# Kernel optimization log

Measured on AMD Instinct MI355X. Metric: run time of the kernel, lower is better.

## Reference

```python
import jax, jax.numpy as jnp
import numpy as np
import math

N_HEAD = 9
N_KV_HEAD = 3
HEAD_DIM = 64
ROPE_THETA = 100000.0


def _rope_cos_sin(seq_len, dim, theta):
    inv_freq = 1.0 / (theta ** (jnp.arange(0, dim, 2, dtype=jnp.float32) / dim))  # (dim//2,)
    t = jnp.arange(seq_len, dtype=jnp.float32)
    ang = jnp.outer(t, inv_freq)  # (T, dim//2)
    return jnp.cos(ang), jnp.sin(ang)


def _apply_rope(x, cos, sin):
    # x: (B, H, T, D); pairs are interleaved along D (torch view_as_complex on (..., D//2, 2))
    B, H, T, D = x.shape
    xr = x.reshape(B, H, T, D // 2, 2)
    x0, x1 = xr[..., 0], xr[..., 1]
    c = cos[None, None, :, :]
    s = sin[None, None, :, :]
    out0 = x0 * c - x1 * s
    out1 = x0 * s + x1 * c
    return jnp.stack([out0, out1], axis=-1).reshape(B, H, T, D)


def setup_inputs() -> dict:
    key = jax.random.key(0)
    ks = jax.random.split(key, 5)
    B, T, C = 4, 2048, 576
    scale_in = 1.0 / math.sqrt(C)
    return {
        "x": jax.random.normal(ks[0], (B, T, C), dtype=jnp.float32),
        "wq": jax.random.normal(ks[1], (N_HEAD * HEAD_DIM, C), dtype=jnp.float32) * scale_in,
        "wk": jax.random.normal(ks[2], (N_KV_HEAD * HEAD_DIM, C), dtype=jnp.float32) * scale_in,
        "wv": jax.random.normal(ks[3], (N_KV_HEAD * HEAD_DIM, C), dtype=jnp.float32) * scale_in,
        "wo": jax.random.normal(ks[4], (C, N_HEAD * HEAD_DIM), dtype=jnp.float32) * scale_in,
    }


def reference(x, wq, wk, wv, wo):
    B, T, C = x.shape
    n_rep = N_HEAD // N_KV_HEAD

    q = (x @ wq.T).reshape(B, T, N_HEAD, HEAD_DIM).transpose(0, 2, 1, 3)      # (B,Hq,T,D)
    k = (x @ wk.T).reshape(B, T, N_KV_HEAD, HEAD_DIM).transpose(0, 2, 1, 3)   # (B,Hkv,T,D)
    v = (x @ wv.T).reshape(B, T, N_KV_HEAD, HEAD_DIM).transpose(0, 2, 1, 3)

    cos, sin = _rope_cos_sin(T, HEAD_DIM, ROPE_THETA)
    q = _apply_rope(q, cos, sin)
    k = _apply_rope(k, cos, sin)

    # GQA: broadcast each KV head across n_rep query heads without materializing copies
    qg = q.reshape(B, N_KV_HEAD, n_rep, T, HEAD_DIM)
    att = jnp.einsum("bgrtd,bgsd->bgrts", qg, k) * (1.0 / math.sqrt(HEAD_DIM))  # (B,Hkv,rep,T,T)
    causal = jnp.tril(jnp.ones((T, T), dtype=bool))
    att = jnp.where(causal[None, None, None, :, :], att, -jnp.inf)
    att = jax.nn.softmax(att, axis=-1)
    y = jnp.einsum("bgrts,bgsd->bgrtd", att, v)                                # (B,Hkv,rep,T,D)
    y = y.reshape(B, N_HEAD, T, HEAD_DIM).transpose(0, 2, 1, 3).reshape(B, T, N_HEAD * HEAD_DIM)
    return y @ wo.T
```

## Files before the change

kernel.cpp:

```cpp
#include <hip/hip_runtime.h>
#include <stdint.h>

typedef __attribute__((ext_vector_type(8))) short bf16x8;
typedef __attribute__((ext_vector_type(16))) float f32x16;

#define MFMA32(a, b, c) __builtin_amdgcn_mfma_f32_32x32x16_bf16(a, b, c, 0, 0, 0)

#define BB 4
#define TT 2048
#define CC 576
#define NH 9
#define NKV 3
#define HD 64
#define MM (BB * TT)
#define NQKV 960

#define QSC 0.18033688011112042f

__device__ __forceinline__ unsigned short f2bf(float f) {
  union { float f; uint32_t u; } v; v.f = f;
  uint32_t u = v.u;
  uint32_t r = (u + 0x7fffu + ((u >> 16) & 1u)) >> 16;
  return (unsigned short)r;
}

__device__ __forceinline__ void gl16(const void* g, void* l) {
  __builtin_amdgcn_global_load_lds(
      (const __attribute__((address_space(1))) unsigned int*)g,
      (__attribute__((address_space(3))) unsigned int*)l, 16, 0, 0);
}

__device__ __forceinline__ float fexp2(float x) {
  float r;
  asm("v_exp_f32 %0, %1" : "=v"(r) : "v"(x));
  return r;
}

__global__ __launch_bounds__(256) void prep_kernel(
    const float* __restrict__ x, const float* __restrict__ wq,
    const float* __restrict__ wk, const float* __restrict__ wv,
    const float* __restrict__ wo,
    unsigned short* __restrict__ xh, unsigned short* __restrict__ wqkv,
    unsigned short* __restrict__ woh, float* __restrict__ tc,
    float* __restrict__ ts) {
  const int NX4 = MM * CC / 4;
  const int NW4 = NQKV * CC / 4;
  const int NO4 = CC * CC / 4;
  const int NT = TT * 32;
  const int total = NX4 + NW4 + NO4 + NT;
  for (int i = blockIdx.x * blockDim.x + threadIdx.x; i < total;
       i += gridDim.x * blockDim.x) {
    if (i < NX4) {
      float4 v = ((const float4*)x)[i];
      ushort4 o;
      o.x = f2bf(v.x); o.y = f2bf(v.y); o.z = f2bf(v.z); o.w = f2bf(v.w);
      ((ushort4*)xh)[i] = o;
    } else if (i < NX4 + NW4) {
      int j = i - NX4;
      int n = (j * 4) / CC;
      const float* src = (n < 576) ? wq + j * 4
                       : (n < 768) ? wk + j * 4 - 576 * CC
                                   : wv + j * 4 - 768 * CC;
      float4 v = *(const float4*)src;
      ushort4 o;
      o.x = f2bf(v.x); o.y = f2bf(v.y); o.z = f2bf(v.z); o.w = f2bf(v.w);
      ((ushort4*)wqkv)[j] = o;
    } else if (i < NX4 + NW4 + NO4) {
      int j = i - NX4 - NW4;
      float4 v = ((const float4*)wo)[j];
      ushort4 o;
      o.x = f2bf(v.x); o.y = f2bf(v.y); o.z = f2bf(v.z); o.w = f2bf(v.w);
      ((ushort4*)woh)[j] = o;
    } else {
      int j = i - NX4 - NW4 - NO4;
      int t = j >> 5, pi = j & 31;
      double invf = pow(100000.0, -(double)(2 * pi) / 64.0);
      double ang = (double)t * invf;
      tc[j] = (float)cos(ang);
      ts[j] = (float)sin(ang);
    }
  }
}

__global__ __launch_bounds__(512, 4) void gemm_qkv(
    const unsigned short* __restrict__ xh, const unsigned short* __restrict__ wqkv,
    const float* __restrict__ tc, const float* __restrict__ ts,
    unsigned short* __restrict__ qb, unsigned short* __restrict__ kst,
    unsigned short* __restrict__ vst) {
  const int l = threadIdx.x & 63, w = threadIdx.x >> 6;
  const int ln = l & 31, hi = l >> 5;
  const int bm = blockIdx.y * 256, bn = blockIdx.x * 64;

  __shared__ unsigned short als[2][16384];
  __shared__ unsigned short bls[2][4096];

  int asrc[4];
#pragma unroll
  for (int i = 0; i < 4; ++i)
    asrc[i] = (bm + w * 32 + i * 8 + (l >> 3)) * CC + ((l & 7) ^ ((l >> 3) & 7)) * 8;
  const int bsrc = (bn + w * 8 + (l >> 3)) * CC + ((l & 7) ^ ((l >> 3) & 7)) * 8;

  f32x16 acc0, acc1;
#pragma unroll
  for (int r = 0; r < 16; ++r) { acc0[r] = 0.f; acc1[r] = 0.f; }

#pragma unroll
  for (int i = 0; i < 4; ++i) gl16(xh + asrc[i], (char*)&als[0][0] + w * 4096 + i * 1024);
  gl16(wqkv + bsrc, (char*)&bls[0][0] + w * 1024);

  int cur = 0;
  for (int t = 0; t < 9; ++t) {
    if (t + 1 < 9) {
      const int k0 = (t + 1) * 64;
#pragma unroll
      for (int i = 0; i < 4; ++i)
        gl16(xh + asrc[i] + k0, (char*)&als[cur ^ 1][0] + w * 4096 + i * 1024);
      gl16(wqkv + bsrc + k0, (char*)&bls[cur ^ 1][0] + w * 1024);
      asm volatile("s_waitcnt vmcnt(5)" ::: "memory");
    } else {
      asm volatile("s_waitcnt vmcnt(0)" ::: "memory");
    }
    __builtin_amdgcn_s_barrier();
    __builtin_amdgcn_sched_barrier(0);

    const char* ab = (const char*)&als[cur][0];
    const char* bb = (const char*)&bls[cur][0];
    __builtin_amdgcn_s_setprio(1);
#pragma unroll
    for (int ks = 0; ks < 4; ++ks) {
      const int ch = (((ks * 2 + hi) ^ (ln & 7)) << 4);
      bf16x8 af = *(const bf16x8*)(ab + (w * 32 + ln) * 128 + ch);
      bf16x8 b0 = *(const bf16x8*)(bb + ln * 128 + ch);
      bf16x8 b1 = *(const bf16x8*)(bb + (32 + ln) * 128 + ch);
      acc0 = MFMA32(af, b0, acc0);
      acc1 = MFMA32(af, b1, acc1);
    }
    __builtin_amdgcn_s_setprio(0);

    __builtin_amdgcn_sched_barrier(0);
    __builtin_amdgcn_s_barrier();
    cur ^= 1;
  }

#pragma unroll
  for (int n32 = 0; n32 < 2; ++n32) {
    const int col = bn + n32 * 32 + ln;
    const int d = col & 63;
#pragma unroll
    for (int r = 0; r < 16; ++r) {
      const int m = bm + w * 32 + (r & 3) + 8 * (r >> 2) + 4 * hi;
      float v = n32 ? acc1[r] : acc0[r];
      float partner = __shfl_xor(v, 1);
      const int bi = m >> 11, t = m & 2047;
      if (col < 768) {
        const int pi = d >> 1;
        const float c = tc[t * 32 + pi], s = ts[t * 32 + pi];
        v = (d & 1) ? (partner * s + v * c) : (v * c - partner * s);
      }
      if (col < 576) {
        const int h = col >> 6;
        qb[(((size_t)bi * NH + h) * TT + t) * HD + d] = f2bf(v * QSC);
      } else if (col < 768) {
        const int h = (col - 576) >> 6;
        const size_t head = (size_t)bi * NKV + h;
        const int tt = t & 63;
        kst[(head * 32 + (t >> 6)) * 4096 + ((d >> 4) * 2 + (tt >> 5)) * 512
            + ((((d >> 3) & 1) << 5) + (tt & 31)) * 8 + (d & 7)] = f2bf(v);
      } else {
        const int h = (col - 768) >> 6;
        const size_t head = (size_t)bi * NKV + h;
        const int tt = t & 63;
        vst[(head * 32 + (t >> 6)) * 4096 + ((tt >> 4) * 2 + (d >> 5)) * 512
            + ((((tt >> 3) & 1) << 5) + (d & 31)) * 8 + (tt & 7)] = f2bf(v);
      }
    }
  }
}

__global__ __launch_bounds__(512) void attn_kernel(
    const unsigned short* __restrict__ qbuf, const unsigned short* __restrict__ kst,
    const unsigned short* __restrict__ vst, unsigned short* __restrict__ yb) {
  const int j = blockIdx.x, kvh = blockIdx.y, b = blockIdx.z;
  const int i = j % 7, hr = j / 7;
  const int h = kvh * 3 + hr;
  const int l = threadIdx.x & 63;
  const int w8 = threadIdx.x >> 6;
  const int g = w8 >> 2;
  const int wq = w8 & 3;
  const int ln = l & 31, hi = l >> 5;
  const size_t head = (size_t)b * NKV + kvh;

  const int qt0 = 15 - i, qt1 = i + 2, qt2 = (i == 5) ? 0 : 1;
  const int m0 = qt0 + 1, m1 = qt1 + 1;
  const int m2 = (i >= 5) ? qt2 + 1 : 0;
  const int m01 = m0 + m1;
  const int tot = m01 + m2;

  __shared__ unsigned short kls[2][3][4096];
  __shared__ unsigned short vls[2][3][4096];
  __shared__ float licomb[256];

  const unsigned short* qptr = qbuf + ((size_t)b * NH + h) * TT * HD;
  const int row0 = qt0 * 128 + wq * 32 + ln;
  const int row1 = qt1 * 128 + wq * 32 + ln;
  const int row2 = qt2 * 128 + wq * 32 + ln;

  bf16x8 qf0[4], qf1[4], qf2[4], qc[4];
#pragma unroll
  for (int ds = 0; ds < 4; ++ds) {
    qf0[ds] = *(const bf16x8*)(qptr + (size_t)row0 * HD + ds * 16 + hi * 8);
    qf1[ds] = *(const bf16x8*)(qptr + (size_t)row1 * HD + ds * 16 + hi * 8);
    qf2[ds] = *(const bf16x8*)(qptr + (size_t)row2 * HD + ds * 16 + hi * 8);
  }
  qc[0] = qf0[0]; qc[1] = qf0[1]; qc[2] = qf0[2]; qc[3] = qf0[3];
  int qt_c = qt0, qrow_c = row0, nt_c = m0;

  const char* kgb = (const char*)(kst + head * 32 * 4096);
  const char* vgb = (const char*)(vst + head * 32 * 4096);

  f32x16 o0, o1, fzero;
  float ls[16];
#pragma unroll
  for (int r = 0; r < 16; ++r) { o0[r] = 0.f; o1[r] = 0.f; ls[r] = 0.f; fzero[r] = 0.f; }

#pragma unroll
  for (int pre = 0; pre < 2; ++pre) {
    const size_t tb = (size_t)(2 * pre + g) * 8192;
#pragma unroll
    for (int i2 = 0; i2 < 2; ++i2) {
      const int off = wq * 2048 + i2 * 1024;
      gl16(kgb + tb + off + l * 16, (char*)&kls[g][pre][0] + off);
      gl16(vgb + tb + off + l * 16, (char*)&vls[g][pre][0] + off);
    }
  }
  asm volatile("s_waitcnt vmcnt(4)" ::: "memory");
  __builtin_amdgcn_s_barrier();
  __builtin_amdgcn_sched_barrier(0);

  int jt = 0;
  int s = 0;

  for (int it = 0; it < tot; ++it) {
    if (it + 2 < tot) {
      const int f = it + 2;
      const int u2 = (f < m0) ? f : ((f < m01) ? f - m0 : f - m01);
      const size_t tb = (size_t)(2 * u2 + g) * 8192;
      char* kl = (char*)&kls[g][(it + 2) % 3][0];
      char* vl = (char*)&vls[g][(it + 2) % 3][0];
#pragma unroll
      for (int i2 = 0; i2 < 2; ++i2) {
        const int off = wq * 2048 + i2 * 1024;
        gl16(kgb + tb + off + l * 16, kl + off);
        gl16(vgb + tb + off + l * 16, vl + off);
      }
    }

    const char* kb = (const char*)&kls[g][it % 3][0];
    const char* vb = (const char*)&vls[g][it % 3][0];

    f32x16 s0, s1;
    __builtin_amdgcn_s_setprio(1);
    {
      bf16x8 k0 = *(const bf16x8*)(kb + 0 * 1024 + l * 16);
      bf16x8 k1 = *(const bf16x8*)(kb + 1 * 1024 + l * 16);
      s0 = MFMA32(k0, qc[0], fzero);
      s1 = MFMA32(k1, qc[0], fzero);
    }
#pragma unroll
    for (int ds = 1; ds < 4; ++ds) {
      bf16x8 k0 = *(const bf16x8*)(kb + (ds * 2 + 0) * 1024 + l * 16);
      bf16x8 k1 = *(const bf16x8*)(kb + (ds * 2 + 1) * 1024 + l * 16);
      s0 = MFMA32(k0, qc[ds], s0);
      s1 = MFMA32(k1, qc[ds], s1);
    }
    __builtin_amdgcn_s_setprio(0);

    const bool segEnd = (jt == qt_c);
    if (segEnd) {
      const int kvt = 2 * qt_c + g;
#pragma unroll
      for (int r = 0; r < 16; ++r) {
        const int kg = kvt * 64 + (r & 3) + 8 * (r >> 2) + 4 * hi;
        if (kg > qrow_c) s0[r] = -1e30f;
        if (kg + 32 > qrow_c) s1[r] = -1e30f;
      }
    }

#pragma unroll
    for (int r = 0; r < 16; ++r) {
      s0[r] = fexp2(s0[r]);
      s1[r] = fexp2(s1[r]);
    }
#pragma unroll
    for (int r = 0; r < 16; ++r) ls[r] += s0[r] + s1[r];

    unsigned int pa[4][4];
#pragma unroll
    for (int t = 0; t < 2; ++t) {
#pragma unroll
      for (int m = 0; m < 2; ++m) {
        float p0 = t ? s1[8 * m + 0] : s0[8 * m + 0];
        float p1 = t ? s1[8 * m + 1] : s0[8 * m + 1];
        float p2 = t ? s1[8 * m + 2] : s0[8 * m + 2];
        float p3 = t ? s1[8 * m + 3] : s0[8 * m + 3];
        float p4 = t ? s1[8 * m + 4] : s0[8 * m + 4];
        float p5 = t ? s1[8 * m + 5] : s0[8 * m + 5];
        float p6 = t ? s1[8 * m + 6] : s0[8 * m + 6];
        float p7 = t ? s1[8 * m + 7] : s0[8 * m + 7];
        unsigned int w0, w1, w2, w3;
        asm("v_cvt_pk_bf16_f32 %0, %1, %2" : "=v"(w0) : "v"(p0), "v"(p1));
        asm("v_cvt_pk_bf16_f32 %0, %1, %2" : "=v"(w1) : "v"(p2), "v"(p3));
        asm("v_cvt_pk_bf16_f32 %0, %1, %2" : "=v"(w2) : "v"(p4), "v"(p5));
        asm("v_cvt_pk_bf16_f32 %0, %1, %2" : "=v"(w3) : "v"(p6), "v"(p7));
        asm("v_permlane32_swap_b32 %0, %1" : "+v"(w0), "+v"(w2));
        asm("v_permlane32_swap_b32 %0, %1" : "+v"(w1), "+v"(w3));
        pa[2 * t + m][0] = w0; pa[2 * t + m][1] = w1;
        pa[2 * t + m][2] = w2; pa[2 * t + m][3] = w3;
      }
    }

    __builtin_amdgcn_s_setprio(1);
#pragma unroll
    for (int ks = 0; ks < 4; ++ks) {
      union { unsigned int u[4]; bf16x8 v; } cvt;
      cvt.u[0] = pa[ks][0]; cvt.u[1] = pa[ks][1];
      cvt.u[2] = pa[ks][2]; cvt.u[3] = pa[ks][3];
      bf16x8 v0 = *(const bf16x8*)(vb + (ks * 2 + 0) * 1024 + l * 16);
      bf16x8 v1 = *(const bf16x8*)(vb + (ks * 2 + 1) * 1024 + l * 16);
      o0 = MFMA32(cvt.v, v0, o0);
      o1 = MFMA32(cvt.v, v1, o1);
    }
    __builtin_amdgcn_s_setprio(0);

    if (segEnd) {
#pragma unroll
      for (int st = 8; st >= 1; st >>= 1)
#pragma unroll
        for (int r = 0; r < 8; ++r)
          if (r < st) ls[r] += ls[r + st];
      const float tm0 = ls[0] + __shfl_xor(ls[0], 32);
      char* chunk;
      {
        const int buf = it % 3;
        chunk = (char*)((wq == 0) ? &kls[0][buf][0]
               : (wq == 1) ? &vls[0][buf][0]
               : (wq == 2) ? &kls[1][buf][0]
                           : &vls[1][buf][0]);
      }
      __syncthreads();
      if (g == 1) {
#pragma unroll
        for (int r = 0; r < 16; ++r) {
          *(float*)(chunk + r * 256 + l * 4) = o0[r];
          *(float*)(chunk + (16 + r) * 256 + l * 4) = o1[r];
        }
        licomb[wq * 64 + l] = tm0;
      }
      __syncthreads();
      if (g == 0) {
#pragma unroll
        for (int r = 0; r < 16; ++r) {
          o0[r] += *(const float*)(chunk + r * 256 + l * 4);
          o1[r] += *(const float*)(chunk + (16 + r) * 256 + l * 4);
        }
        const float li = tm0 + licomb[wq * 64 + l];
        const float inv = 1.0f / li;
#pragma unroll
        for (int r = 0; r < 16; ++r) {
          const int cr = (r & 3) + 8 * (r >> 2) + 4 * hi;
          const float ir = __shfl(inv, cr);
          const int t = qt_c * 128 + wq * 32 + cr;
          unsigned short* yp = yb + ((size_t)b * TT + t) * CC + h * HD;
          yp[ln] = f2bf(o0[r] * ir);
          yp[32 + ln] = f2bf(o1[r] * ir);
        }
      }
#pragma unroll
      for (int r = 0; r < 16; ++r) { o0[r] = 0.f; o1[r] = 0.f; ls[r] = 0.f; }
    }

    __builtin_amdgcn_sched_barrier(0);
    if (it + 2 < tot) {
      asm volatile("s_waitcnt vmcnt(4)" ::: "memory");
    } else {
      asm volatile("s_waitcnt vmcnt(0)" ::: "memory");
    }
    __builtin_amdgcn_s_barrier();
    __builtin_amdgcn_sched_barrier(0);

    ++jt;
    if (jt == nt_c) {
      jt = 0; ++s;
      if (s == 1) {
        qt_c = qt1; qrow_c = row1; nt_c = m1;
        qc[0] = qf1[0]; qc[1] = qf1[1]; qc[2] = qf1[2]; qc[3] = qf1[3];
      } else {
        qt_c = qt2; qrow_c = row2; nt_c = m2;
        qc[0] = qf2[0]; qc[1] = qf2[1]; qc[2] = qf2[2]; qc[3] = qf2[3];
      }
    }
  }
}

__global__ __launch_bounds__(512, 4) void gemm_out(
    const unsigned short* __restrict__ yb, const unsigned short* __restrict__ woh,
    float* __restrict__ out) {
  const int l = threadIdx.x & 63, w = threadIdx.x >> 6;
  const int ln = l & 31, hi = l >> 5;
  const int bm = blockIdx.y * 256, bn = blockIdx.x * 64;

  __shared__ unsigned short als[2][16384];
  __shared__ unsigned short bls[2][4096];

  int asrc[4];
#pragma unroll
  for (int i = 0; i < 4; ++i)
    asrc[i] = (bm + w * 32 + i * 8 + (l >> 3)) * CC + ((l & 7) ^ ((l >> 3) & 7)) * 8;
  const int bsrc = (bn + w * 8 + (l >> 3)) * CC + ((l & 7) ^ ((l >> 3) & 7)) * 8;

  f32x16 acc0, acc1;
#pragma unroll
  for (int r = 0; r < 16; ++r) { acc0[r] = 0.f; acc1[r] = 0.f; }

#pragma unroll
  for (int i = 0; i < 4; ++i) gl16(yb + asrc[i], (char*)&als[0][0] + w * 4096 + i * 1024);
  gl16(woh + bsrc, (char*)&bls[0][0] + w * 1024);

  int cur = 0;
  for (int t = 0; t < 9; ++t) {
    if (t + 1 < 9) {
      const int k0 = (t + 1) * 64;
#pragma unroll
      for (int i = 0; i < 4; ++i)
        gl16(yb + asrc[i] + k0, (char*)&als[cur ^ 1][0] + w * 4096 + i * 1024);
      gl16(woh + bsrc + k0, (char*)&bls[cur ^ 1][0] + w * 1024);
      asm volatile("s_waitcnt vmcnt(5)" ::: "memory");
    } else {
      asm volatile("s_waitcnt vmcnt(0)" ::: "memory");
    }
    __builtin_amdgcn_s_barrier();
    __builtin_amdgcn_sched_barrier(0);

    const char* ab = (const char*)&als[cur][0];
    const char* bb = (const char*)&bls[cur][0];
    __builtin_amdgcn_s_setprio(1);
#pragma unroll
    for (int ks = 0; ks < 4; ++ks) {
      const int ch = (((ks * 2 + hi) ^ (ln & 7)) << 4);
      bf16x8 af = *(const bf16x8*)(ab + (w * 32 + ln) * 128 + ch);
      bf16x8 b0 = *(const bf16x8*)(bb + ln * 128 + ch);
      bf16x8 b1 = *(const bf16x8*)(bb + (32 + ln) * 128 + ch);
      acc0 = MFMA32(af, b0, acc0);
      acc1 = MFMA32(af, b1, acc1);
    }
    __builtin_amdgcn_s_setprio(0);

    __builtin_amdgcn_sched_barrier(0);
    __builtin_amdgcn_s_barrier();
    cur ^= 1;
  }

#pragma unroll
  for (int n32 = 0; n32 < 2; ++n32) {
    const int col = bn + n32 * 32 + ln;
#pragma unroll
    for (int r = 0; r < 16; ++r) {
      const int m = bm + w * 32 + (r & 3) + 8 * (r >> 2) + 4 * hi;
      out[(size_t)m * CC + col] = n32 ? acc1[r] : acc0[r];
    }
  }
}

extern "C" void kernel_launch(void* const* d_in, const int* in_sizes, int n_in,
                              void* d_out, int out_size, void* d_ws, size_t ws_size,
                              hipStream_t stream) {
  const float* x = (const float*)d_in[0];
  const float* wq = (const float*)d_in[1];
  const float* wk = (const float*)d_in[2];
  const float* wv = (const float*)d_in[3];
  const float* wo = (const float*)d_in[4];
  float* out = (float*)d_out;

  char* ws = (char*)d_ws;
  unsigned short* xh = (unsigned short*)ws;    ws += (size_t)MM * CC * 2;
  unsigned short* wqkv = (unsigned short*)ws;  ws += (size_t)NQKV * CC * 2;
  unsigned short* woh = (unsigned short*)ws;   ws += (size_t)CC * CC * 2;
  float* tc = (float*)ws;                      ws += (size_t)TT * 32 * 4;
  float* tsn = (float*)ws;                     ws += (size_t)TT * 32 * 4;
  unsigned short* qbuf = (unsigned short*)ws;  ws += (size_t)BB * NH * TT * HD * 2;
  unsigned short* kst = (unsigned short*)ws;   ws += (size_t)BB * NKV * TT * HD * 2;
  unsigned short* vst = (unsigned short*)ws;   ws += (size_t)BB * NKV * HD * TT * 2;
  unsigned short* yb = (unsigned short*)ws;    ws += (size_t)MM * CC * 2;

  prep_kernel<<<dim3(2048), dim3(256), 0, stream>>>(x, wq, wk, wv, wo, xh, wqkv, woh, tc, tsn);
  gemm_qkv<<<dim3(NQKV / 64, MM / 256), dim3(512), 0, stream>>>(xh, wqkv, tc, tsn, qbuf, kst, vst);
  attn_kernel<<<dim3(21, NKV, BB), dim3(512), 0, stream>>>(qbuf, kst, vst, yb);
  gemm_out<<<dim3(CC / 64, MM / 256), dim3(512), 0, stream>>>(yb, woh, out);
}
```

Baseline: 100.2 us.

## Rebalance causal attention work into more blocks with double-buffered KV tiles

The attention grid grows from 21 to 39 blocks per (kv-head, batch). Each block now handles one large query tile, and three of them also take one small tile, instead of packing up to three query tiles into one block. The KV prefetch pipeline drops from triple to double buffering, which cuts shared memory per block, and launch bounds now request 4 blocks per CU for higher occupancy. The trade-off is a shallower prefetch depth, so load latency is less well hidden, and per-block balance is more uneven.

```diff
diff --git a/kernel.cpp b/kernel.cpp
--- a/kernel.cpp
+++ b/kernel.cpp
@@ -177,11 +177,11 @@
   }
 }
 
-__global__ __launch_bounds__(512) void attn_kernel(
+__global__ __launch_bounds__(512, 4) void attn_kernel(
     const unsigned short* __restrict__ qbuf, const unsigned short* __restrict__ kst,
     const unsigned short* __restrict__ vst, unsigned short* __restrict__ yb) {
-  const int j = blockIdx.x, kvh = blockIdx.y, b = blockIdx.z;
-  const int i = j % 7, hr = j / 7;
+  const int jx = blockIdx.x, kvh = blockIdx.y, b = blockIdx.z;
+  const int j = jx % 13, hr = jx / 13;
   const int h = kvh * 3 + hr;
   const int l = threadIdx.x & 63;
   const int w8 = threadIdx.x >> 6;
@@ -190,27 +190,25 @@
   const int ln = l & 31, hi = l >> 5;
   const size_t head = (size_t)b * NKV + kvh;
 
-  const int qt0 = 15 - i, qt1 = i + 2, qt2 = (i == 5) ? 0 : 1;
-  const int m0 = qt0 + 1, m1 = qt1 + 1;
-  const int m2 = (i >= 5) ? qt2 + 1 : 0;
-  const int m01 = m0 + m1;
-  const int tot = m01 + m2;
-
-  __shared__ unsigned short kls[2][3][4096];
-  __shared__ unsigned short vls[2][3][4096];
+  const int qt0 = 15 - j;
+  const int qt1 = (j >= 9 && j <= 11) ? (j - 9) : -1;
+  const int m0 = qt0 + 1;
+  const int m1 = (qt1 >= 0) ? qt1 + 1 : 0;
+  const int tot = m0 + m1;
+
+  __shared__ unsigned short kls[2][2][4096];
+  __shared__ unsigned short vls[2][2][4096];
   __shared__ float licomb[256];
 
   const unsigned short* qptr = qbuf + ((size_t)b * NH + h) * TT * HD;
   const int row0 = qt0 * 128 + wq * 32 + ln;
-  const int row1 = qt1 * 128 + wq * 32 + ln;
-  const int row2 = qt2 * 128 + wq * 32 + ln;
-
-  bf16x8 qf0[4], qf1[4], qf2[4], qc[4];
+  const int row1 = ((qt1 >= 0) ? qt1 : 0) * 128 + wq * 32 + ln;
+
+  bf16x8 qf0[4], qf1[4], qc[4];
 #pragma unroll
   for (int ds = 0; ds < 4; ++ds) {
     qf0[ds] = *(const bf16x8*)(qptr + (size_t)row0 * HD + ds * 16 + hi * 8);
     qf1[ds] = *(const bf16x8*)(qptr + (size_t)row1 * HD + ds * 16 + hi * 8);
-    qf2[ds] = *(const bf16x8*)(qptr + (size_t)row2 * HD + ds * 16 + hi * 8);
   }
   qc[0] = qf0[0]; qc[1] = qf0[1]; qc[2] = qf0[2]; qc[3] = qf0[3];
   int qt_c = qt0, qrow_c = row0, nt_c = m0;
@@ -223,40 +221,40 @@
 #pragma unroll
   for (int r = 0; r < 16; ++r) { o0[r] = 0.f; o1[r] = 0.f; ls[r] = 0.f; fzero[r] = 0.f; }
 
-#pragma unroll
-  for (int pre = 0; pre < 2; ++pre) {
-    const size_t tb = (size_t)(2 * pre + g) * 8192;
+  {
+    const size_t tb = (size_t)g * 8192;
 #pragma unroll
     for (int i2 = 0; i2 < 2; ++i2) {
       const int off = wq * 2048 + i2 * 1024;
-      gl16(kgb + tb + off + l * 16, (char*)&kls[g][pre][0] + off);
-      gl16(vgb + tb + off + l * 16, (char*)&vls[g][pre][0] + off);
-    }
-  }
-  asm volatile("s_waitcnt vmcnt(4)" ::: "memory");
-  __builtin_amdgcn_s_barrier();
-  __builtin_amdgcn_sched_barrier(0);
+      gl16(kgb + tb + off + l * 16, (char*)&kls[g][0][0] + off);
+      gl16(vgb + tb + off + l * 16, (char*)&vls[g][0][0] + off);
+    }
+  }
 
   int jt = 0;
-  int s = 0;
 
   for (int it = 0; it < tot; ++it) {
-    if (it + 2 < tot) {
-      const int f = it + 2;
-      const int u2 = (f < m0) ? f : ((f < m01) ? f - m0 : f - m01);
-      const size_t tb = (size_t)(2 * u2 + g) * 8192;
-      char* kl = (char*)&kls[g][(it + 2) % 3][0];
-      char* vl = (char*)&vls[g][(it + 2) % 3][0];
+    if (it + 1 < tot) {
+      const int f = it + 1;
+      const int u = (f < m0) ? f : f - m0;
+      const size_t tb = (size_t)(2 * u + g) * 8192;
+      char* kl = (char*)&kls[g][(it + 1) & 1][0];
+      char* vl = (char*)&vls[g][(it + 1) & 1][0];
 #pragma unroll
       for (int i2 = 0; i2 < 2; ++i2) {
         const int off = wq * 2048 + i2 * 1024;
         gl16(kgb + tb + off + l * 16, kl + off);
         gl16(vgb + tb + off + l * 16, vl + off);
       }
-    }
-
-    const char* kb = (const char*)&kls[g][it % 3][0];
-    const char* vb = (const char*)&vls[g][it % 3][0];
+      asm volatile("s_waitcnt vmcnt(4)" ::: "memory");
+    } else {
+      asm volatile("s_waitcnt vmcnt(0)" ::: "memory");
+    }
+    __builtin_amdgcn_s_barrier();
+    __builtin_amdgcn_sched_barrier(0);
+
+    const char* kb = (const char*)&kls[g][it & 1][0];
+    const char* vb = (const char*)&vls[g][it & 1][0];
 
     f32x16 s0, s1;
     __builtin_amdgcn_s_setprio(1);
@@ -341,7 +339,7 @@
       const float tm0 = ls[0] + __shfl_xor(ls[0], 32);
       char* chunk;
       {
-        const int buf = it % 3;
+        const int buf = it & 1;
         chunk = (char*)((wq == 0) ? &kls[0][buf][0]
                : (wq == 1) ? &vls[0][buf][0]
                : (wq == 2) ? &kls[1][buf][0]
@@ -380,24 +378,14 @@
     }
 
     __builtin_amdgcn_sched_barrier(0);
-    if (it + 2 < tot) {
-      asm volatile("s_waitcnt vmcnt(4)" ::: "memory");
-    } else {
-      asm volatile("s_waitcnt vmcnt(0)" ::: "memory");
-    }
     __builtin_amdgcn_s_barrier();
     __builtin_amdgcn_sched_barrier(0);
 
     ++jt;
-    if (jt == nt_c) {
-      jt = 0; ++s;
-      if (s == 1) {
-        qt_c = qt1; qrow_c = row1; nt_c = m1;
-        qc[0] = qf1[0]; qc[1] = qf1[1]; qc[2] = qf1[2]; qc[3] = qf1[3];
-      } else {
-        qt_c = qt2; qrow_c = row2; nt_c = m2;
-        qc[0] = qf2[0]; qc[1] = qf2[1]; qc[2] = qf2[2]; qc[3] = qf2[3];
-      }
+    if (jt == nt_c && it + 1 < tot) {
+      jt = 0;
+      qt_c = qt1; qrow_c = row1; nt_c = m1;
+      qc[0] = qf1[0]; qc[1] = qf1[1]; qc[2] = qf1[2]; qc[3] = qf1[3];
     }
   }
 }
@@ -494,6 +482,6 @@
 
   prep_kernel<<<dim3(2048), dim3(256), 0, stream>>>(x, wq, wk, wv, wo, xh, wqkv, woh, tc, tsn);
   gemm_qkv<<<dim3(NQKV / 64, MM / 256), dim3(512), 0, stream>>>(xh, wqkv, tc, tsn, qbuf, kst, vst);
-  attn_kernel<<<dim3(21, NKV, BB), dim3(512), 0, stream>>>(qbuf, kst, vst, yb);
+  attn_kernel<<<dim3(39, NKV, BB), dim3(512), 0, stream>>>(qbuf, kst, vst, yb);
   gemm_out<<<dim3(CC / 64, MM / 256), dim3(512), 0, stream>>>(yb, woh, out);
 }
```

New measurement: 98.93 us. About the same (-1.2%).
